# Kernel optimization log

Measured on AMD Instinct MI355X. Metric: run time of the kernel, lower is better.

## Reference

```python
import jax, jax.numpy as jnp
import numpy as np
import math

B, N, D, H, NBT = 16, 512, 512, 8, 5
HD = D // H
EPS = 1e-5

def _ln(x, g, b):
    mu = jnp.mean(x, axis=-1, keepdims=True)
    var = jnp.mean(jnp.square(x - mu), axis=-1, keepdims=True)
    return (x - mu) * jax.lax.rsqrt(var + EPS) * g + b

def setup_inputs() -> dict:
    key = jax.random.key(0)
    ks = jax.random.split(key, 16)
    s = 0.02
    inp = {
        'x': jax.random.normal(ks[0], (B, N, D), jnp.float32),
        'adj': jax.random.randint(ks[1], (B, N, N), 0, NBT, jnp.int64),
        'mask': (jax.random.uniform(ks[2], (B, N)) > 0.1).astype(jnp.float32),
        'Wq': jax.random.normal(ks[3], (D, D), jnp.float32) * s,
        'bq': jnp.zeros((D,), jnp.float32),
        'Wk': jax.random.normal(ks[4], (D, D), jnp.float32) * s,
        'bk': jnp.zeros((D,), jnp.float32),
        'Wv': jax.random.normal(ks[5], (D, D), jnp.float32) * s,
        'bv': jnp.zeros((D,), jnp.float32),
        'Wo': jax.random.normal(ks[6], (D, D), jnp.float32) * s,
        'bo': jnp.zeros((D,), jnp.float32),
        'edge_bias': jax.random.normal(ks[7], (NBT, H), jnp.float32) * s,
        'W1': jax.random.normal(ks[8], (D, 4 * D), jnp.float32) * s,
        'b1': jnp.zeros((4 * D,), jnp.float32),
        'W2': jax.random.normal(ks[9], (4 * D, D), jnp.float32) * s,
        'b2': jnp.zeros((D,), jnp.float32),
        'g1': jnp.ones((D,), jnp.float32),
        'beta1': jnp.zeros((D,), jnp.float32),
        'g2': jnp.ones((D,), jnp.float32),
        'beta2': jnp.zeros((D,), jnp.float32),
    }
    return inp

def reference(x, adj, mask, Wq, bq, Wk, bk, Wv, bv, Wo, bo, edge_bias,
              W1, b1, W2, b2, g1, beta1, g2, beta2):
    # --- attention block ---
    residual = x
    h = _ln(x, g1, beta1)
    # (B,N,D) -> (B,H,N,HD)
    Q = (h @ Wq + bq).reshape(B, N, H, HD).transpose(0, 2, 1, 3)
    K = (h @ Wk + bk).reshape(B, N, H, HD).transpose(0, 2, 1, 3)
    V = (h @ Wv + bv).reshape(B, N, H, HD).transpose(0, 2, 1, 3)
    attn = jnp.einsum('bhqd,bhkd->bhqk', Q, K) / math.sqrt(HD)
    # per-head edge-type bias: gather (B,N,N,H) -> (B,H,N,N)
    eb = edge_bias[adj].transpose(0, 3, 1, 2)
    attn = attn + eb
    mask_2d = mask[:, None, None, :] * mask[:, None, :, None]  # (B,1,N,N)
    attn = jnp.where(mask_2d == 0, -jnp.inf, attn)
    attn = jax.nn.softmax(attn, axis=-1)
    attn = jnp.nan_to_num(attn, nan=0.0)  # fully-masked rows -> 0
    out = jnp.einsum('bhqk,bhkd->bhqd', attn, V)
    out = out.transpose(0, 2, 1, 3).reshape(B, N, D)
    out = out @ Wo + bo
    x = residual + out  # dropout is identity in eval
    # --- FFN block ---
    residual = x
    h = _ln(x, g2, beta2)
    h = jax.nn.gelu(h @ W1 + b1, approximate=False) @ W2 + b2
    x = residual + h
    return x * mask[:, :, None]
```

## Files before the change

kernel.cpp:

```cpp
#include <hip/hip_runtime.h>
#include <hip/hip_bf16.h>
#include <math.h>
#include <stdint.h>

typedef __hip_bfloat16 bf16;
typedef __bf16 bf16x8 __attribute__((ext_vector_type(8)));
typedef float f32x4 __attribute__((ext_vector_type(4)));

#define MFMA16 __builtin_amdgcn_mfma_f32_16x16x32_bf16
#define L2E 1.4426950408889634f

__device__ __forceinline__ void gll16(const void* gsrc, void* ldst) {
  __builtin_amdgcn_global_load_lds(
      (const __attribute__((address_space(1))) unsigned int*)(uintptr_t)gsrc,
      (__attribute__((address_space(3))) unsigned int*)(uintptr_t)ldst,
      16, 0, 0);
}

__global__ __launch_bounds__(256) void pack_adj(const int* __restrict__ adj,
                                                const float* __restrict__ mask,
                                                unsigned char* __restrict__ out) {
  size_t i0 = ((size_t)blockIdx.x * 256 + threadIdx.x) * 16;
  int b = (int)(i0 >> 18);
  int k0 = (int)(i0 & 511);
  const float* mb = mask + b * 512 + k0;
  const int* ap = adj + i0;
  unsigned char o16[16];
#pragma unroll
  for (int j = 0; j < 16; ++j) {
    o16[j] = (unsigned char)(ap[j] | (mb[j] == 0.f ? 0x80 : 0));
  }
  *(uint4*)(out + i0) = *(const uint4*)o16;
}

__global__ __launch_bounds__(256) void transpose_wt6(
    const float* __restrict__ s0, const float* __restrict__ s1,
    const float* __restrict__ s2, const float* __restrict__ s3,
    const float* __restrict__ s4, const float* __restrict__ s5,
    bf16* __restrict__ d0, bf16* __restrict__ d1, bf16* __restrict__ d2,
    bf16* __restrict__ d3, bf16* __restrict__ d4, bf16* __restrict__ d5) {
  __shared__ float t[32][33];
  const int bid = blockIdx.x;
  const float* W;
  bf16* Wt;
  int K, N, n0, k0;
  if (bid < 1024) {
    int mi = bid >> 8, tt = bid & 255;
    W = (mi == 0) ? s0 : (mi == 1) ? s1 : (mi == 2) ? s2 : s3;
    Wt = (mi == 0) ? d0 : (mi == 1) ? d1 : (mi == 2) ? d2 : d3;
    K = 512; N = 512; n0 = (tt & 15) * 32; k0 = (tt >> 4) * 32;
  } else if (bid < 2048) {
    int tt = bid - 1024;
    W = s4; Wt = d4; K = 512; N = 2048;
    n0 = (tt & 63) * 32; k0 = (tt >> 6) * 32;
  } else {
    int tt = bid - 2048;
    W = s5; Wt = d5; K = 2048; N = 512;
    n0 = (tt & 15) * 32; k0 = (tt >> 4) * 32;
  }
  int tx = threadIdx.x, ty = threadIdx.y;
#pragma unroll
  for (int s = 0; s < 32; s += 8) t[ty + s][tx] = W[(size_t)(k0 + ty + s) * N + n0 + tx];
  __syncthreads();
#pragma unroll
  for (int s = 0; s < 32; s += 8) Wt[(size_t)(n0 + ty + s) * K + k0 + tx] = (bf16)t[tx][ty + s];
}

__global__ __launch_bounds__(256) void ln_k(const float* __restrict__ x,
                                            const float* __restrict__ gam,
                                            const float* __restrict__ bet,
                                            bf16* __restrict__ out) {
  int l = threadIdx.x & 63, w = threadIdx.x >> 6;
  size_t row = (size_t)blockIdx.x * 4 + w;
  const float* xr = x + row * 512 + l * 8;
  float4 v0 = *(const float4*)xr;
  float4 v1 = *(const float4*)(xr + 4);
  float s = v0.x + v0.y + v0.z + v0.w + v1.x + v1.y + v1.z + v1.w;
  float q = v0.x * v0.x + v0.y * v0.y + v0.z * v0.z + v0.w * v0.w +
            v1.x * v1.x + v1.y * v1.y + v1.z * v1.z + v1.w * v1.w;
#pragma unroll
  for (int o = 1; o < 64; o <<= 1) { s += __shfl_xor(s, o); q += __shfl_xor(q, o); }
  float mean = s * (1.0f / 512.0f);
  float var = q * (1.0f / 512.0f) - mean * mean;
  float rstd = rsqrtf(var + 1e-5f);
  const float* gr = gam + l * 8;
  const float* br = bet + l * 8;
  float4 ga = *(const float4*)gr, gb = *(const float4*)(gr + 4);
  float4 ba = *(const float4*)br, bb = *(const float4*)(br + 4);
  bf16 t8[8];
  t8[0] = (bf16)((v0.x - mean) * rstd * ga.x + ba.x);
  t8[1] = (bf16)((v0.y - mean) * rstd * ga.y + ba.y);
  t8[2] = (bf16)((v0.z - mean) * rstd * ga.z + ba.z);
  t8[3] = (bf16)((v0.w - mean) * rstd * ga.w + ba.w);
  t8[4] = (bf16)((v1.x - mean) * rstd * gb.x + bb.x);
  t8[5] = (bf16)((v1.y - mean) * rstd * gb.y + bb.y);
  t8[6] = (bf16)((v1.z - mean) * rstd * gb.z + bb.z);
  t8[7] = (bf16)((v1.w - mean) * rstd * gb.w + bb.w);
  *(uint4*)(out + row * 512 + l * 8) = *(const uint4*)t8;
}

template <int MODE, int BM, int BN>
__global__ __launch_bounds__(256) void gemm_bt(
    const bf16* __restrict__ A, const bf16* __restrict__ Bt, int M, int N, int K,
    const float* __restrict__ b0, const float* __restrict__ b1p,
    const float* __restrict__ b2p, const float* __restrict__ resid,
    const float* __restrict__ mrow, float* __restrict__ outF,
    bf16* __restrict__ outH, bf16* __restrict__ outV) {
  constexpr int RA = BM / 32, RB = BN / 32;
  __shared__ __align__(16) bf16 Asw[2][BM * 64];
  __shared__ __align__(16) bf16 Bsw[2][BN * 64];
  const int tid = threadIdx.x;
  const int l = tid & 63, w = tid >> 6;
  const int g = l >> 4, ln = l & 15;
  const int wm = w >> 1, wn = w & 1;
  const int m0 = blockIdx.x * BM, n0 = blockIdx.y * BN;

  f32x4 acc[RA][RB];
  f32x4 zero = {0.f, 0.f, 0.f, 0.f};
#pragma unroll
  for (int i = 0; i < RA; ++i)
#pragma unroll
    for (int j = 0; j < RB; ++j) acc[i][j] = zero;

  const bf16* aSrc[RA];
  const bf16* bSrc[RB];
#pragma unroll
  for (int rr = 0; rr < RA; ++rr) {
    int m = w * (BM / 4) + rr * 8 + (l >> 3);
    int gs = (l & 7) ^ (m & 7);
    aSrc[rr] = A + (size_t)(m0 + m) * K + gs * 8;
  }
#pragma unroll
  for (int rr = 0; rr < RB; ++rr) {
    int n = w * (BN / 4) + rr * 8 + (l >> 3);
    int gs = (l & 7) ^ (n & 7);
    bSrc[rr] = Bt + (size_t)(n0 + n) * K + gs * 8;
  }

  const int NT = K >> 6;
#pragma unroll
  for (int rr = 0; rr < RA; ++rr) gll16(aSrc[rr], &Asw[0][w * (BM * 16) + rr * 512]);
#pragma unroll
  for (int rr = 0; rr < RB; ++rr) gll16(bSrc[rr], &Bsw[0][w * (BN * 16) + rr * 512]);
  __syncthreads();

  for (int ti = 0; ti < NT; ++ti) {
    const int cur = ti & 1, nxt = cur ^ 1;
    if (ti + 1 < NT) {
      const int kt = (ti + 1) << 6;
#pragma unroll
      for (int rr = 0; rr < RA; ++rr)
        gll16(aSrc[rr] + kt, &Asw[nxt][w * (BM * 16) + rr * 512]);
#pragma unroll
      for (int rr = 0; rr < RB; ++rr)
        gll16(bSrc[rr] + kt, &Bsw[nxt][w * (BN * 16) + rr * 512]);
    }
#pragma unroll
    for (int kk = 0; kk < 2; ++kk) {
      bf16x8 af[RA], bfr[RB];
#pragma unroll
      for (int mt = 0; mt < RA; ++mt) {
        int m = wm * (BM / 2) + mt * 16 + ln;
        af[mt] = *(const bf16x8*)&Asw[cur][m * 64 + (((kk * 4 + g) ^ (m & 7)) * 8)];
      }
#pragma unroll
      for (int nt = 0; nt < RB; ++nt) {
        int n = wn * (BN / 2) + nt * 16 + ln;
        bfr[nt] = *(const bf16x8*)&Bsw[cur][n * 64 + (((kk * 4 + g) ^ (n & 7)) * 8)];
      }
#pragma unroll
      for (int mt = 0; mt < RA; ++mt)
#pragma unroll
        for (int nt = 0; nt < RB; ++nt)
          acc[mt][nt] = MFMA16(af[mt], bfr[nt], acc[mt][nt], 0, 0, 0);
    }
    __syncthreads();
  }

#pragma unroll
  for (int mt = 0; mt < RA; ++mt) {
#pragma unroll
    for (int nt = 0; nt < RB; ++nt) {
      if (MODE == 0) {
        const int gn = n0 + wn * (BN / 2) + nt * 16 + ln;
        const int which = gn >> 9;
        const int dm = gn & 511;
        const int hh = dm >> 6, hd = dm & 63;
        const float bias = (which == 0) ? b0[dm] : ((which == 1) ? b1p[dm] : b2p[dm]);
        const int gm0 = m0 + wm * (BM / 2) + mt * 16 + g * 4;
        const int bq = gm0 >> 9, qq0 = gm0 & 511;
        if (which == 2) {
          bf16 t4[4];
#pragma unroll
          for (int r = 0; r < 4; ++r) t4[r] = (bf16)(acc[mt][nt][r] + bias);
          *(uint2*)&outV[(((size_t)(bq * 8 + hh)) * 64 + hd) * 512 + qq0] =
              *(const uint2*)t4;
        } else {
#pragma unroll
          for (int r = 0; r < 4; ++r) {
            float v = acc[mt][nt][r] + bias;
            if (which == 0) v *= 0.125f * L2E;
            outH[(size_t)which * 4194304 + (((size_t)(bq * 8 + hh)) * 512 + qq0 + r) * 64 + hd] =
                (bf16)v;
          }
        }
      } else {
#pragma unroll
        for (int r = 0; r < 4; ++r) {
          int gm = m0 + wm * (BM / 2) + mt * 16 + g * 4 + r;
          int gn = n0 + wn * (BN / 2) + nt * 16 + ln;
          float v = acc[mt][nt][r];
          if (MODE == 1) {
            v += b0[gn] + resid[(size_t)gm * 512 + gn];
            outF[(size_t)gm * 512 + gn] = v;
          } else if (MODE == 2) {
            v += b0[gn];
            v = 0.5f * v * (1.0f + erff(v * 0.70710678118f));
            outH[(size_t)gm * 2048 + gn] = (bf16)v;
          } else {
            v += b0[gn] + resid[(size_t)gm * 512 + gn];
            v *= mrow[gm];
            outF[(size_t)gm * 512 + gn] = v;
          }
        }
      }
    }
  }
}

__global__ __launch_bounds__(256, 4) void attn_k(
    const bf16* __restrict__ Qg, const bf16* __restrict__ Kg,
    const bf16* __restrict__ Vtg, const unsigned char* __restrict__ adj8,
    const float* __restrict__ mask, const float* __restrict__ ebias,
    bf16* __restrict__ out) {
  __shared__ __align__(16) bf16 Ksw[2][64 * 64];
  __shared__ __align__(16) bf16 Vt[2][64 * 64];
  __shared__ __align__(16) bf16 Pb[4][16 * 64];
  const int tid = threadIdx.x;
  const int l = tid & 63, w = tid >> 6, g = l >> 4, ln = l & 15;
  const int bh = blockIdx.y, b = bh >> 3, h = bh & 7;
  const int qt = blockIdx.x;
  const bf16* kb = Kg + (size_t)bh * 512 * 64;
  const bf16* vtb = Vtg + (size_t)bh * 64 * 512;

  int ksrc_off[2], vtsrc_off[2];
#pragma unroll
  for (int rr = 0; rr < 2; ++rr) {
    int m = w * 16 + rr * 8 + (l >> 3);
    int gs = (l & 7) ^ (l >> 3);
    ksrc_off[rr] = m * 64 + gs * 8;
    vtsrc_off[rr] = m * 512 + gs * 8;
  }

  const int qrow = qt * 64 + w * 16 + ln;
  const bf16* qp = Qg + ((size_t)bh * 512 + qrow) * 64;
  bf16x8 qf0 = *(const bf16x8*)(qp + g * 8);
  bf16x8 qf1 = *(const bf16x8*)(qp + 32 + g * 8);

  const bool rowlive = mask[b * 512 + qrow] != 0.f;
  float e0 = ebias[0 * 8 + h] * L2E, e1 = ebias[1 * 8 + h] * L2E;
  float e2 = ebias[2 * 8 + h] * L2E, e3 = ebias[3 * 8 + h] * L2E;
  float e4 = ebias[4 * 8 + h] * L2E;
  const unsigned char* adjq = adj8 + ((size_t)b * 512 + qrow) * 512;

  f32x4 zero = {0.f, 0.f, 0.f, 0.f};
  f32x4 o[4];
#pragma unroll
  for (int dt = 0; dt < 4; ++dt) o[dt] = zero;
  float rsum = 0.f;
  bf16* pw = &Pb[w][0];

#pragma unroll
  for (int rr = 0; rr < 2; ++rr) {
    gll16(kb + ksrc_off[rr], &Ksw[0][w * 1024 + rr * 512]);
    gll16(vtb + vtsrc_off[rr], &Vt[0][w * 1024 + rr * 512]);
  }
  uchar4 c4[4];
#pragma unroll
  for (int t4 = 0; t4 < 4; ++t4) c4[t4] = *(const uchar4*)(adjq + t4 * 16 + g * 4);
  __syncthreads();

  for (int t = 0; t < 8; ++t) {
    const int cur = t & 1, nxt = cur ^ 1;
    uchar4 n4[4];
    if (t < 7) {
      const bf16* kbt = kb + (t + 1) * 4096;
      const bf16* vbt = vtb + (t + 1) * 64;
#pragma unroll
      for (int rr = 0; rr < 2; ++rr) {
        gll16(kbt + ksrc_off[rr], &Ksw[nxt][w * 1024 + rr * 512]);
        gll16(vbt + vtsrc_off[rr], &Vt[nxt][w * 1024 + rr * 512]);
      }
#pragma unroll
      for (int t4 = 0; t4 < 4; ++t4)
        n4[t4] = *(const uchar4*)(adjq + (t + 1) * 64 + t4 * 16 + g * 4);
    }

    f32x4 s[4];
#pragma unroll
    for (int t4 = 0; t4 < 4; ++t4) {
      int kr = t4 * 16 + ln;
      s[t4] = zero;
      bf16x8 a0 = *(const bf16x8*)&Ksw[cur][kr * 64 + ((g ^ (ln & 7)) * 8)];
      s[t4] = MFMA16(a0, qf0, s[t4], 0, 0, 0);
      bf16x8 a1 = *(const bf16x8*)&Ksw[cur][kr * 64 + (((4 + g) ^ (ln & 7)) * 8)];
      s[t4] = MFMA16(a1, qf1, s[t4], 0, 0, 0);
    }

#pragma unroll
    for (int t4 = 0; t4 < 4; ++t4) {
      unsigned char cv[4] = {c4[t4].x, c4[t4].y, c4[t4].z, c4[t4].w};
      bf16 hb[4];
#pragma unroll
      for (int r = 0; r < 4; ++r) {
        int a = cv[r] & 7;
        float eb = (a == 0) ? e0 : (a == 1) ? e1 : (a == 2) ? e2 : (a == 3) ? e3 : e4;
        float p = (!rowlive || (cv[r] & 0x80))
                      ? 0.f
                      : __builtin_amdgcn_exp2f(s[t4][r] + eb);
        rsum += p;
        hb[r] = (bf16)p;
      }
      int sub = t4 * 2 + (g >> 1);
      *(uint2*)&pw[ln * 64 + ((sub ^ (ln & 7)) * 8) + (g & 1) * 4] = *(const uint2*)hb;
    }

#pragma unroll
    for (int ks = 0; ks < 2; ++ks) {
      bf16x8 pa = *(const bf16x8*)&pw[ln * 64 + (((ks * 4 + g) ^ (ln & 7)) * 8)];
#pragma unroll
      for (int dt = 0; dt < 4; ++dt) {
        int d = dt * 16 + ln;
        bf16x8 vvv = *(const bf16x8*)&Vt[cur][d * 64 + (((ks * 4 + g) ^ (d & 7)) * 8)];
        o[dt] = MFMA16(pa, vvv, o[dt], 0, 0, 0);
      }
    }
    __syncthreads();
    if (t < 7) {
#pragma unroll
      for (int t4 = 0; t4 < 4; ++t4) c4[t4] = n4[t4];
    }
  }

  rsum += __shfl_xor(rsum, 16);
  rsum += __shfl_xor(rsum, 32);
  float inv = (rsum > 0.f) ? 1.f / rsum : 0.f;
  const int qbase = qt * 64 + w * 16;
#pragma unroll
  for (int r = 0; r < 4; ++r) {
    float invr = __shfl(inv, g * 4 + r);
#pragma unroll
    for (int dt = 0; dt < 4; ++dt) {
      int q = qbase + g * 4 + r;
      out[((size_t)b * 512 + q) * 512 + h * 64 + dt * 16 + ln] = (bf16)(o[dt][r] * invr);
    }
  }
}

extern "C" void kernel_launch(void* const* d_in, const int* in_sizes, int n_in,
                              void* d_out, int out_size, void* d_ws, size_t ws_size,
                              hipStream_t stream) {
  const float* x = (const float*)d_in[0];
  const int* adj = (const int*)d_in[1];
  const float* mask = (const float*)d_in[2];
  const float* Wq = (const float*)d_in[3];
  const float* bq = (const float*)d_in[4];
  const float* Wk = (const float*)d_in[5];
  const float* bk = (const float*)d_in[6];
  const float* Wv = (const float*)d_in[7];
  const float* bv = (const float*)d_in[8];
  const float* Wo = (const float*)d_in[9];
  const float* bo = (const float*)d_in[10];
  const float* ebias = (const float*)d_in[11];
  const float* W1 = (const float*)d_in[12];
  const float* b1 = (const float*)d_in[13];
  const float* W2 = (const float*)d_in[14];
  const float* b2 = (const float*)d_in[15];
  const float* g1 = (const float*)d_in[16];
  const float* be1 = (const float*)d_in[17];
  const float* g2 = (const float*)d_in[18];
  const float* be2 = (const float*)d_in[19];
  float* outp = (float*)d_out;

  char* ws = (char*)d_ws;
  size_t off = 0;
  auto alloc = [&](size_t bytes) {
    void* p = ws + off;
    off += (bytes + 255) & ~(size_t)255;
    return p;
  };
  const size_t QSZ = 4194304;
  bf16* h1 = (bf16*)alloc(8192UL * 512 * 2);
  bf16* wqkv = (bf16*)alloc(1536UL * 512 * 2);
  bf16* wo_t = (bf16*)alloc(512UL * 512 * 2);
  bf16* w1_t = (bf16*)alloc(2048UL * 512 * 2);
  bf16* w2_t = (bf16*)alloc(512UL * 2048 * 2);
  bf16* qkv = (bf16*)alloc(2UL * QSZ * 2);
  bf16* vt = (bf16*)alloc(QSZ * 2);
  bf16* aout = (bf16*)alloc(8192UL * 512 * 2);
  float* xmid = (float*)alloc(8192UL * 512 * 4);
  bf16* h2 = (bf16*)alloc(8192UL * 512 * 2);
  bf16* a1 = (bf16*)alloc(8192UL * 2048 * 2);
  unsigned char* adj8 = (unsigned char*)alloc(4194304UL);
  if (off > ws_size) return;

  pack_adj<<<1024, 256, 0, stream>>>(adj, mask, adj8);
  transpose_wt6<<<3072, dim3(32, 8), 0, stream>>>(Wq, Wk, Wv, Wo, W1, W2, wqkv,
                                                  wqkv + 512 * 512, wqkv + 1024 * 512,
                                                  wo_t, w1_t, w2_t);

  ln_k<<<2048, 256, 0, stream>>>(x, g1, be1, h1);
  gemm_bt<0, 128, 128><<<dim3(64, 12), 256, 0, stream>>>(
      h1, wqkv, 8192, 1536, 512, bq, bk, bv, nullptr, nullptr, nullptr, qkv, vt);
  attn_k<<<dim3(8, 128), 256, 0, stream>>>(qkv, qkv + QSZ, vt, adj8, mask, ebias, aout);
  gemm_bt<1, 64, 64><<<dim3(128, 8), 256, 0, stream>>>(
      aout, wo_t, 8192, 512, 512, bo, nullptr, nullptr, x, nullptr, xmid, nullptr,
      nullptr);
  ln_k<<<2048, 256, 0, stream>>>(xmid, g2, be2, h2);
  gemm_bt<2, 128, 128><<<dim3(64, 16), 256, 0, stream>>>(
      h2, w1_t, 8192, 2048, 512, b1, nullptr, nullptr, nullptr, nullptr, nullptr, a1,
      nullptr);
  gemm_bt<3, 64, 64><<<dim3(128, 8), 256, 0, stream>>>(
      a1, w2_t, 8192, 512, 2048, b2, nullptr, nullptr, xmid, mask, outp, nullptr,
      nullptr);
}
```

Measured before the change: 153.9 us.

## Stage V-transpose epilogue through LDS and reorder attention grid

In the QKV GEMM, blocks that produce V (blockIdx.y >= 8) now write their accumulator tile into swizzled shared memory. They then read it back so each thread emits 16-byte coalesced stores of the transposed V, replacing scattered 8-byte strided stores. The attention launch grid is also swapped so consecutive blocks map to different (batch, head) pairs for the same query tile, changing scheduling order and L2 locality. The cost is an extra LDS round trip and barrier in the V blocks.

Measured after the change: 147.7 us. 1.04x faster.

```diff
diff --git a/kernel.cpp b/kernel.cpp
--- a/kernel.cpp
+++ b/kernel.cpp
@@ -177,6 +177,41 @@
     __syncthreads();
   }
 
+  if (MODE == 0 && blockIdx.y >= 8) {
+    bf16* lt = &Asw[0][0];
+    const int by = blockIdx.y;
+#pragma unroll
+    for (int nt = 0; nt < RB; ++nt) {
+      const int col = wn * 64 + nt * 16 + ln;
+      const int dm = (by - 8) * 128 + col;
+      const float bias = b2p[dm];
+#pragma unroll
+      for (int mt = 0; mt < RA; ++mt) {
+        const int gr_w = wm * 16 + mt * 4 + g;
+        bf16 t4[4];
+#pragma unroll
+        for (int r = 0; r < 4; ++r) t4[r] = (bf16)(acc[mt][nt][r] + bias);
+        *(uint2*)&lt[col * 128 + ((gr_w ^ (col & 7)) << 2)] = *(const uint2*)t4;
+      }
+    }
+    __syncthreads();
+    const int bq = blockIdx.x >> 2;
+    const int qq0 = (blockIdx.x & 3) * 128;
+    const int l16 = tid & 15;
+#pragma unroll
+    for (int j = 0; j < 8; ++j) {
+      const int col = (tid >> 4) + j * 16;
+      const int gr = l16 * 2;
+      uint2 u0 = *(const uint2*)&lt[col * 128 + (((gr) ^ (col & 7)) << 2)];
+      uint2 u1 = *(const uint2*)&lt[col * 128 + (((gr + 1) ^ (col & 7)) << 2)];
+      uint4 u;
+      u.x = u0.x; u.y = u0.y; u.z = u1.x; u.w = u1.y;
+      const int hh = 2 * (by - 8) + (col >> 6), hd = col & 63;
+      *(uint4*)&outV[(((size_t)(bq * 8 + hh)) * 64 + hd) * 512 + qq0 + l16 * 8] = u;
+    }
+    return;
+  }
+
 #pragma unroll
   for (int mt = 0; mt < RA; ++mt) {
 #pragma unroll
@@ -186,23 +221,15 @@
         const int which = gn >> 9;
         const int dm = gn & 511;
         const int hh = dm >> 6, hd = dm & 63;
-        const float bias = (which == 0) ? b0[dm] : ((which == 1) ? b1p[dm] : b2p[dm]);
+        const float bias = (which == 0) ? b0[dm] : b1p[dm];
         const int gm0 = m0 + wm * (BM / 2) + mt * 16 + g * 4;
         const int bq = gm0 >> 9, qq0 = gm0 & 511;
-        if (which == 2) {
-          bf16 t4[4];
-#pragma unroll
-          for (int r = 0; r < 4; ++r) t4[r] = (bf16)(acc[mt][nt][r] + bias);
-          *(uint2*)&outV[(((size_t)(bq * 8 + hh)) * 64 + hd) * 512 + qq0] =
-              *(const uint2*)t4;
-        } else {
-#pragma unroll
-          for (int r = 0; r < 4; ++r) {
-            float v = acc[mt][nt][r] + bias;
-            if (which == 0) v *= 0.125f * L2E;
-            outH[(size_t)which * 4194304 + (((size_t)(bq * 8 + hh)) * 512 + qq0 + r) * 64 + hd] =
-                (bf16)v;
-          }
+#pragma unroll
+        for (int r = 0; r < 4; ++r) {
+          float v = acc[mt][nt][r] + bias;
+          if (which == 0) v *= 0.125f * L2E;
+          outH[(size_t)which * 4194304 + (((size_t)(bq * 8 + hh)) * 512 + qq0 + r) * 64 + hd] =
+              (bf16)v;
         }
       } else {
 #pragma unroll
@@ -238,8 +265,10 @@
   __shared__ __align__(16) bf16 Pb[4][16 * 64];
   const int tid = threadIdx.x;
   const int l = tid & 63, w = tid >> 6, g = l >> 4, ln = l & 15;
-  const int bh = blockIdx.y, b = bh >> 3, h = bh & 7;
-  const int qt = blockIdx.x;
+  const int bhx = blockIdx.x;
+  const int b = bhx & 15, h = bhx >> 4;
+  const int bh = b * 8 + h;
+  const int qt = blockIdx.y;
   const bf16* kb = Kg + (size_t)bh * 512 * 64;
   const bf16* vtb = Vtg + (size_t)bh * 64 * 512;
 
@@ -412,7 +441,7 @@
   ln_k<<<2048, 256, 0, stream>>>(x, g1, be1, h1);
   gemm_bt<0, 128, 128><<<dim3(64, 12), 256, 0, stream>>>(
       h1, wqkv, 8192, 1536, 512, bq, bk, bv, nullptr, nullptr, nullptr, qkv, vt);
-  attn_k<<<dim3(8, 128), 256, 0, stream>>>(qkv, qkv + QSZ, vt, adj8, mask, ebias, aout);
+  attn_k<<<dim3(128, 8), 256, 0, stream>>>(qkv, qkv + QSZ, vt, adj8, mask, ebias, aout);
   gemm_bt<1, 64, 64><<<dim3(128, 8), 256, 0, stream>>>(
       aout, wo_t, 8192, 512, 512, bo, nullptr, nullptr, x, nullptr, xmid, nullptr,
       nullptr);
```
